# Kernel optimization log

Hardware: AMD Instinct MI355X
Metric: run time of the kernel (lower is better)

Reference implementation:

```python
import jax, jax.numpy as jnp
import numpy as np

B, S, VOCAB = 16384, 50, 100000
EMB = 20
RAW_FEAT = 109            # channel 0 = item id, 108 float features
D = EMB + (RAW_FEAT - 1)  # 128
H = 4 * D                 # 512, pooled concat width
N_BLOCKS = 10
OUT = 20


def setup_inputs() -> dict:
    key = jax.random.key(0)
    ks = jax.random.split(key, 12)
    ids = jax.random.randint(ks[0], (B, S), 0, VOCAB).astype(jnp.float32)
    feats = jax.random.normal(ks[1], (B, S, RAW_FEAT - 1), dtype=jnp.float32)
    inp = jnp.concatenate([ids[:, :, None], feats], axis=2)
    # prefix validity mask with seq_len in [1, S]
    seq_len = jax.random.randint(ks[2], (B,), 1, S + 1)
    mask = (jnp.arange(S)[None, :] < seq_len[:, None]).astype(jnp.int64)
    embed = jax.random.normal(ks[3], (VOCAB, EMB), dtype=jnp.float32) * 0.02
    s1 = 1.0 / np.sqrt(H)
    s2 = 1.0 / np.sqrt(4 * H)
    W1 = jax.random.uniform(ks[4], (N_BLOCKS, H, 4 * H), minval=-s1, maxval=s1)
    b1 = jax.random.uniform(ks[5], (N_BLOCKS, 4 * H), minval=-s1, maxval=s1)
    W2 = jax.random.uniform(ks[6], (N_BLOCKS, 4 * H, H), minval=-s2, maxval=s2)
    b2 = jax.random.uniform(ks[7], (N_BLOCKS, H), minval=-s2, maxval=s2)
    Wf = jax.random.uniform(ks[8], (H, OUT), minval=-s1, maxval=s1)
    bf = jax.random.uniform(ks[9], (OUT,), minval=-s1, maxval=s1)
    return {"input": inp, "mask": mask, "embed": embed, "W1": W1, "b1": b1,
            "W2": W2, "b2": b2, "Wf": Wf, "bf": bf}


def reference(input, mask, embed, W1, b1, W2, b2, Wf, bf):
    ids = input[:, :, 0].astype(jnp.int32)
    x = jnp.concatenate([embed[ids], input[:, :, 1:]], axis=2)  # [B,S,D]
    next_item = x[:, -1, :]                                      # [B,D]
    seq_len = jnp.sum(mask, axis=1)                              # [B]
    valid = (jnp.arange(x.shape[1])[None, :] < seq_len[:, None])[:, :, None]
    # masked mean / max / min over the valid prefix (vectorized)
    denom = seq_len[:, None].astype(x.dtype)
    avg = jnp.sum(jnp.where(valid, x, 0.0), axis=1) / denom
    mx = jnp.clip(jnp.max(jnp.where(valid, x, -jnp.inf), axis=1), 1e-9, 1e9)
    mn = jnp.clip(jnp.min(jnp.where(valid, x, jnp.inf), axis=1), 1e-9, 1e9)
    h = jnp.concatenate([avg, mx, mn, next_item], axis=1)        # [B,4D]
    for i in range(W1.shape[0]):  # 10 residual widen blocks (dropout=eval identity)
        t = jax.nn.relu(h @ W1[i] + b1[i])
        t = jax.nn.relu(t @ W2[i] + b2[i])
        h = h + t
    return h @ Wf + bf
```

## Files before the change

### kernel.cpp

```cpp
#include <hip/hip_runtime.h>
#include <stdint.h>

typedef unsigned short ushort_t;
typedef __attribute__((ext_vector_type(8))) __bf16 bf16x8;
typedef __attribute__((ext_vector_type(4))) float f32x4;

#define B_SZ 16384
#define SEQ 50
#define RAWF 109
#define EMB 20
#define DFEAT 128
#define H 512
#define H4 2048
#define NBLK 10
#define OUTD 20

__device__ __forceinline__ ushort_t f2bf(float f) {
    union { float f; uint32_t u; } v; v.f = f;
    uint32_t r = (v.u + 0x7fffu + ((v.u >> 16) & 1u)) >> 16;
    return (ushort_t)r;
}

__global__ __launch_bounds__(256)
void transpose_bf16_kernel(const float* __restrict__ src, ushort_t* __restrict__ dst,
                           int K, int N) {
    __shared__ float tile[32][33];
    const int i = blockIdx.z;
    const float* s = src + (size_t)i * K * N;
    ushort_t* d = dst + (size_t)i * K * N;
    const int tx = threadIdx.x, ty = threadIdx.y;
    const int k0 = blockIdx.y * 32, n0 = blockIdx.x * 32;
#pragma unroll
    for (int r = 0; r < 4; ++r)
        tile[ty + r * 8][tx] = s[(size_t)(k0 + ty + r * 8) * N + n0 + tx];
    __syncthreads();
#pragma unroll
    for (int r = 0; r < 4; ++r) {
        int n = ty + r * 8;
        d[(size_t)(n0 + n) * K + k0 + tx] = f2bf(tile[tx][n]);
    }
}

__global__ __launch_bounds__(256)
void len_kernel(const int* __restrict__ mask, int* __restrict__ len) {
    const int wid = (blockIdx.x * 256 + threadIdx.x) >> 6;
    const int lane = threadIdx.x & 63;
    if (wid >= B_SZ) return;
    int c = (lane < SEQ) ? mask[(size_t)wid * SEQ + lane] : 0;
#pragma unroll
    for (int off = 32; off > 0; off >>= 1) c += __shfl_down(c, off);
    c = __shfl(c, 0);
    if (lane == 0) len[wid] = c;
}

__global__ __launch_bounds__(128)
void rawfeat_kernel(const float* __restrict__ inp, const int* __restrict__ len,
                    float* __restrict__ hf, ushort_t* __restrict__ hb,
                    int* __restrict__ ids) {
    const int b = blockIdx.x;
    const int jj = threadIdx.x;
    const float* src = inp + (size_t)b * SEQ * RAWF;
    const int L = len[b];
    const bool active = jj < RAWF;
    float sum = 0.f, mx = -3.0e38f, mn = 3.0e38f, nxt = 0.f;
#pragma unroll 5
    for (int s = 0; s < SEQ; ++s) {
        float v = active ? src[s * RAWF + jj] : 0.f;
        if (s < L) { sum += v; mx = fmaxf(mx, v); mn = fminf(mn, v); }
        if (s == SEQ - 1) nxt = v;
        if (jj == 0) ids[(size_t)b * SEQ + s] = (int)v;
    }
    if (jj >= 1 && jj < RAWF) {
        const int j = 19 + jj;
        const float avg = sum / (float)L;
        mx = fminf(fmaxf(mx, 1e-9f), 1e9f);
        mn = fminf(fmaxf(mn, 1e-9f), 1e9f);
        const size_t base = (size_t)b * H;
        hf[base + j] = avg;             hb[base + j] = f2bf(avg);
        hf[base + DFEAT + j] = mx;      hb[base + DFEAT + j] = f2bf(mx);
        hf[base + 2 * DFEAT + j] = mn;  hb[base + 2 * DFEAT + j] = f2bf(mn);
        hf[base + 3 * DFEAT + j] = nxt; hb[base + 3 * DFEAT + j] = f2bf(nxt);
    }
}

__global__ __launch_bounds__(256)
void embfeat_kernel(const int* __restrict__ ids, const int* __restrict__ len,
                    const float* __restrict__ embed,
                    float* __restrict__ hf, ushort_t* __restrict__ hb) {
    const int x = threadIdx.x & 31;
    const int row = (blockIdx.x * 256 + threadIdx.x) >> 5;
    if (row >= B_SZ) return;
    const int L = len[row];
    const int* idrow = ids + (size_t)row * SEQ;
    const bool act = x < EMB;
    float sum = 0.f, mx = -3.0e38f, mn = 3.0e38f, nxt = 0.f;
#pragma unroll 5
    for (int s = 0; s < SEQ; ++s) {
        const int id = idrow[s];
        const float v = act ? embed[(size_t)id * EMB + x] : 0.f;
        if (s < L) { sum += v; mx = fmaxf(mx, v); mn = fminf(mn, v); }
        if (s == SEQ - 1) nxt = v;
    }
    if (act) {
        const float avg = sum / (float)L;
        mx = fminf(fmaxf(mx, 1e-9f), 1e9f);
        mn = fminf(fmaxf(mn, 1e-9f), 1e9f);
        const size_t base = (size_t)row * H;
        hf[base + x] = avg;             hb[base + x] = f2bf(avg);
        hf[base + DFEAT + x] = mx;      hb[base + DFEAT + x] = f2bf(mx);
        hf[base + 2 * DFEAT + x] = mn;  hb[base + 2 * DFEAT + x] = f2bf(mn);
        hf[base + 3 * DFEAT + x] = nxt; hb[base + 3 * DFEAT + x] = f2bf(nxt);
    }
}

template <int MODE>
__global__ __launch_bounds__(256, 2)
void gemm_kernel(const ushort_t* __restrict__ A, const ushort_t* __restrict__ Bt,
                 const float* __restrict__ bias,
                 ushort_t* __restrict__ outBf,
                 float* __restrict__ hf, ushort_t* __restrict__ hb,
                 int M, int N, int K) {
    __shared__ alignas(16) ushort_t lA[128 * 64];
    __shared__ alignas(16) ushort_t lB[128 * 64];
    const int tid = threadIdx.x;
    const int lane = tid & 63;
    const int w = tid >> 6;
    const int wm = w >> 1, wn = w & 1;

    const int gx = N >> 7;
    const int nwg = (M >> 7) * gx;
    const int cpx = nwg >> 3;
    const int bid = blockIdx.x;
    const int wg = (bid & 7) * cpx + (bid >> 3);
    const int ntile = wg % gx, mtile = wg / gx;

    const ushort_t* Abase = A + (size_t)mtile * 128 * K;
    const ushort_t* Bbase = Bt + (size_t)ntile * 128 * K;

    f32x4 acc[4][4];
#pragma unroll
    for (int a = 0; a < 4; ++a)
#pragma unroll
        for (int b = 0; b < 4; ++b) acc[a][b] = (f32x4)(0.f);

    const int l3 = lane >> 3;
    const int c16 = lane & 7;
    const int cl = c16 ^ l3;
    const int frow = lane & 15;
    const int k16b = lane >> 4;

    const int nkt = K >> 6;
    for (int kt = 0; kt < nkt; ++kt) {
#pragma unroll
        for (int it = 0; it < 4; ++it) {
            const int row = w * 32 + it * 8 + l3;
            const ushort_t* ga = Abase + (size_t)row * K + kt * 64 + cl * 8;
            const ushort_t* gb = Bbase + (size_t)row * K + kt * 64 + cl * 8;
            __builtin_amdgcn_global_load_lds(
                (const __attribute__((address_space(1))) void*)ga,
                (__attribute__((address_space(3))) void*)(lA + (w * 32 + it * 8) * 64),
                16, 0, 0);
            __builtin_amdgcn_global_load_lds(
                (const __attribute__((address_space(1))) void*)gb,
                (__attribute__((address_space(3))) void*)(lB + (w * 32 + it * 8) * 64),
                16, 0, 0);
        }
        asm volatile("s_waitcnt vmcnt(0)" ::: "memory");
        __syncthreads();

        bf16x8 af[4][2], bfg[4][2];
#pragma unroll
        for (int mf = 0; mf < 4; ++mf)
#pragma unroll
            for (int ks = 0; ks < 2; ++ks) {
                const int row = wm * 64 + mf * 16 + frow;
                const int c = (ks * 4 + k16b) ^ (row & 7);
                af[mf][ks] = *(const bf16x8*)(lA + row * 64 + c * 8);
            }
#pragma unroll
        for (int nf = 0; nf < 4; ++nf)
#pragma unroll
            for (int ks = 0; ks < 2; ++ks) {
                const int row = wn * 64 + nf * 16 + frow;
                const int c = (ks * 4 + k16b) ^ (row & 7);
                bfg[nf][ks] = *(const bf16x8*)(lB + row * 64 + c * 8);
            }
#pragma unroll
        for (int mf = 0; mf < 4; ++mf)
#pragma unroll
            for (int nf = 0; nf < 4; ++nf)
#pragma unroll
                for (int ks = 0; ks < 2; ++ks)
                    acc[mf][nf] = __builtin_amdgcn_mfma_f32_16x16x32_bf16(
                        af[mf][ks], bfg[nf][ks], acc[mf][nf], 0, 0, 0);
        __syncthreads();
    }

#pragma unroll
    for (int mf = 0; mf < 4; ++mf)
#pragma unroll
        for (int nf = 0; nf < 4; ++nf) {
            const int row0 = mtile * 128 + wm * 64 + mf * 16 + (lane >> 4) * 4;
            const int col = ntile * 128 + wn * 64 + nf * 16 + (lane & 15);
            const float bcol = bias[col];
#pragma unroll
            for (int jj = 0; jj < 4; ++jj) {
                float v = acc[mf][nf][jj] + bcol;
                v = v > 0.f ? v : 0.f;
                const size_t idx = (size_t)(row0 + jj) * N + col;
                if (MODE == 0) {
                    outBf[idx] = f2bf(v);
                } else {
                    float nh = hf[idx] + v;
                    hf[idx] = nh;
                    hb[idx] = f2bf(nh);
                }
            }
        }
}

__global__ __launch_bounds__(256)
void final_kernel(const float* __restrict__ hf, const float* __restrict__ Wf,
                  const float* __restrict__ bfv, float* __restrict__ out) {
    const int gid = blockIdx.x * 256 + threadIdx.x;
    if (gid >= B_SZ * OUTD) return;
    const int b = gid / OUTD, o = gid % OUTD;
    const float* hrow = hf + (size_t)b * H;
    float acc = bfv[o];
    for (int k = 0; k < H; ++k) acc += hrow[k] * Wf[k * OUTD + o];
    out[gid] = acc;
}

extern "C" void kernel_launch(void* const* d_in, const int* in_sizes, int n_in,
                              void* d_out, int out_size, void* d_ws, size_t ws_size,
                              hipStream_t stream) {
    const float* inp   = (const float*)d_in[0];
    const int*   mask  = (const int*)d_in[1];
    const float* embed = (const float*)d_in[2];
    const float* W1    = (const float*)d_in[3];
    const float* b1    = (const float*)d_in[4];
    const float* W2    = (const float*)d_in[5];
    const float* b2    = (const float*)d_in[6];
    const float* Wf    = (const float*)d_in[7];
    const float* bfv   = (const float*)d_in[8];
    float* out = (float*)d_out;

    char* ws = (char*)d_ws;
    ushort_t* W1t = (ushort_t*)ws;
    ushort_t* W2t = W1t + (size_t)NBLK * H4 * H;
    float*    hf  = (float*)(W2t + (size_t)NBLK * H * H4);
    ushort_t* hb  = (ushort_t*)(hf + (size_t)B_SZ * H);
    ushort_t* T   = hb + (size_t)B_SZ * H;
    int* ids = (int*)T;
    int* lenb = ids + (size_t)B_SZ * SEQ;

    transpose_bf16_kernel<<<dim3(H4 / 32, H / 32, NBLK), dim3(32, 8), 0, stream>>>(W1, W1t, H, H4);
    transpose_bf16_kernel<<<dim3(H / 32, H4 / 32, NBLK), dim3(32, 8), 0, stream>>>(W2, W2t, H4, H);

    len_kernel<<<(B_SZ * 64 + 255) / 256, 256, 0, stream>>>(mask, lenb);
    rawfeat_kernel<<<B_SZ, 128, 0, stream>>>(inp, lenb, hf, hb, ids);
    embfeat_kernel<<<(B_SZ * 32 + 255) / 256, 256, 0, stream>>>(ids, lenb, embed, hf, hb);

    for (int i = 0; i < NBLK; ++i) {
        gemm_kernel<0><<<(B_SZ / 128) * (H4 / 128), 256, 0, stream>>>(
            hb, W1t + (size_t)i * H4 * H, b1 + (size_t)i * H4, T, nullptr, nullptr,
            B_SZ, H4, H);
        gemm_kernel<1><<<(B_SZ / 128) * (H / 128), 256, 0, stream>>>(
            T, W2t + (size_t)i * H * H4, b2 + (size_t)i * H, nullptr, hf, hb,
            B_SZ, H, H4);
    }

    final_kernel<<<(B_SZ * OUTD + 255) / 256, 256, 0, stream>>>(hf, Wf, bfv, out);
}
```

Before: 1.307 ms.

## Double-buffer LDS in GEMM with 256x128 tiles and eight waves

```diff
diff --git a/kernel.cpp b/kernel.cpp
--- a/kernel.cpp
+++ b/kernel.cpp
@@ -114,27 +114,28 @@
 }
 
 template <int MODE>
-__global__ __launch_bounds__(256, 2)
+__global__ __launch_bounds__(512, 2)
 void gemm_kernel(const ushort_t* __restrict__ A, const ushort_t* __restrict__ Bt,
                  const float* __restrict__ bias,
                  ushort_t* __restrict__ outBf,
                  float* __restrict__ hf, ushort_t* __restrict__ hb,
                  int M, int N, int K) {
-    __shared__ alignas(16) ushort_t lA[128 * 64];
-    __shared__ alignas(16) ushort_t lB[128 * 64];
+    __shared__ alignas(16) ushort_t lA[2][256 * 64];
+    __shared__ alignas(16) ushort_t lB[2][128 * 64];
     const int tid = threadIdx.x;
     const int lane = tid & 63;
     const int w = tid >> 6;
-    const int wm = w >> 1, wn = w & 1;
+    const int wm = w >> 1;
+    const int wn = w & 1;
 
     const int gx = N >> 7;
-    const int nwg = (M >> 7) * gx;
+    const int nwg = (M >> 8) * gx;
     const int cpx = nwg >> 3;
     const int bid = blockIdx.x;
     const int wg = (bid & 7) * cpx + (bid >> 3);
     const int ntile = wg % gx, mtile = wg / gx;
 
-    const ushort_t* Abase = A + (size_t)mtile * 128 * K;
+    const ushort_t* Abase = A + (size_t)mtile * 256 * K;
     const ushort_t* Bbase = Bt + (size_t)ntile * 128 * K;
 
     f32x4 acc[4][4];
@@ -144,38 +145,51 @@
         for (int b = 0; b < 4; ++b) acc[a][b] = (f32x4)(0.f);
 
     const int l3 = lane >> 3;
-    const int c16 = lane & 7;
-    const int cl = c16 ^ l3;
+    const int cl = (lane & 7) ^ l3;
     const int frow = lane & 15;
     const int k16b = lane >> 4;
 
-    const int nkt = K >> 6;
-    for (int kt = 0; kt < nkt; ++kt) {
+    auto stage = [&](int bi, int kt) {
+        const int koff = kt * 64;
+        ushort_t* la = lA[bi];
+        ushort_t* lb = lB[bi];
 #pragma unroll
         for (int it = 0; it < 4; ++it) {
             const int row = w * 32 + it * 8 + l3;
-            const ushort_t* ga = Abase + (size_t)row * K + kt * 64 + cl * 8;
-            const ushort_t* gb = Bbase + (size_t)row * K + kt * 64 + cl * 8;
+            const ushort_t* ga = Abase + (size_t)row * K + koff + cl * 8;
             __builtin_amdgcn_global_load_lds(
                 (const __attribute__((address_space(1))) void*)ga,
-                (__attribute__((address_space(3))) void*)(lA + (w * 32 + it * 8) * 64),
+                (__attribute__((address_space(3))) void*)(la + (w * 32 + it * 8) * 64),
                 16, 0, 0);
+        }
+#pragma unroll
+        for (int it = 0; it < 2; ++it) {
+            const int row = w * 16 + it * 8 + l3;
+            const ushort_t* gb = Bbase + (size_t)row * K + koff + cl * 8;
             __builtin_amdgcn_global_load_lds(
                 (const __attribute__((address_space(1))) void*)gb,
-                (__attribute__((address_space(3))) void*)(lB + (w * 32 + it * 8) * 64),
+                (__attribute__((address_space(3))) void*)(lb + (w * 16 + it * 8) * 64),
                 16, 0, 0);
         }
-        asm volatile("s_waitcnt vmcnt(0)" ::: "memory");
-        __syncthreads();
-
-        bf16x8 af[4][2], bfg[4][2];
+    };
+
+    const int nkt = K >> 6;
+    stage(0, 0);
+    asm volatile("s_waitcnt vmcnt(0)" ::: "memory");
+    __syncthreads();
+
+    for (int kt = 0; kt < nkt; ++kt) {
+        const int cur = kt & 1;
+        if (kt + 1 < nkt) stage(cur ^ 1, kt + 1);
+
+        bf16x8 af[4][2], bfr[4][2];
 #pragma unroll
         for (int mf = 0; mf < 4; ++mf)
 #pragma unroll
             for (int ks = 0; ks < 2; ++ks) {
                 const int row = wm * 64 + mf * 16 + frow;
                 const int c = (ks * 4 + k16b) ^ (row & 7);
-                af[mf][ks] = *(const bf16x8*)(lA + row * 64 + c * 8);
+                af[mf][ks] = *(const bf16x8*)(lA[cur] + row * 64 + c * 8);
             }
 #pragma unroll
         for (int nf = 0; nf < 4; ++nf)
@@ -183,8 +197,10 @@
             for (int ks = 0; ks < 2; ++ks) {
                 const int row = wn * 64 + nf * 16 + frow;
                 const int c = (ks * 4 + k16b) ^ (row & 7);
-                bfg[nf][ks] = *(const bf16x8*)(lB + row * 64 + c * 8);
+                bfr[nf][ks] = *(const bf16x8*)(lB[cur] + row * 64 + c * 8);
             }
+
+        __builtin_amdgcn_s_setprio(1);
 #pragma unroll
         for (int mf = 0; mf < 4; ++mf)
 #pragma unroll
@@ -192,15 +208,20 @@
 #pragma unroll
                 for (int ks = 0; ks < 2; ++ks)
                     acc[mf][nf] = __builtin_amdgcn_mfma_f32_16x16x32_bf16(
-                        af[mf][ks], bfg[nf][ks], acc[mf][nf], 0, 0, 0);
-        __syncthreads();
+                        af[mf][ks], bfr[nf][ks], acc[mf][nf], 0, 0, 0);
+        __builtin_amdgcn_s_setprio(0);
+
+        if (kt + 1 < nkt) {
+            asm volatile("s_waitcnt vmcnt(0)" ::: "memory");
+            __syncthreads();
+        }
     }
 
 #pragma unroll
     for (int mf = 0; mf < 4; ++mf)
 #pragma unroll
         for (int nf = 0; nf < 4; ++nf) {
-            const int row0 = mtile * 128 + wm * 64 + mf * 16 + (lane >> 4) * 4;
+            const int row0 = mtile * 256 + wm * 64 + mf * 16 + (lane >> 4) * 4;
             const int col = ntile * 128 + wn * 64 + nf * 16 + (lane & 15);
             const float bcol = bias[col];
 #pragma unroll
@@ -262,10 +283,10 @@
     embfeat_kernel<<<(B_SZ * 32 + 255) / 256, 256, 0, stream>>>(ids, lenb, embed, hf, hb);
 
     for (int i = 0; i < NBLK; ++i) {
-        gemm_kernel<0><<<(B_SZ / 128) * (H4 / 128), 256, 0, stream>>>(
+        gemm_kernel<0><<<(B_SZ / 256) * (H4 / 128), 512, 0, stream>>>(
             hb, W1t + (size_t)i * H4 * H, b1 + (size_t)i * H4, T, nullptr, nullptr,
             B_SZ, H4, H);
-        gemm_kernel<1><<<(B_SZ / 128) * (H / 128), 256, 0, stream>>>(
+        gemm_kernel<1><<<(B_SZ / 256) * (H / 128), 512, 0, stream>>>(
             T, W2t + (size_t)i * H * H4, b2 + (size_t)i * H, nullptr, hf, hb,
             B_SZ, H, H4);
     }
```

Measured after the change: 1.560 ms. 1.19x slower.
